# Kernel optimization log

Measured on AMD Instinct MI355X. Metric: run time of the kernel, lower is better.

Reference implementation:

```python
import jax, jax.numpy as jnp
import numpy as np


def setup_inputs() -> dict:
    key = jax.random.key(0)
    k1, k2, k3, k4 = jax.random.split(key, 4)
    T, IN, OUT = 4096, 4096, 4096  # tokens, in_features, out_features
    x = jax.random.normal(k1, (T, IN), dtype=jnp.float32)
    # simulated FP8 weight values (already quantized integers-ish codes stored as float)
    weight = jax.random.normal(k2, (OUT, IN), dtype=jnp.float32)
    # per-output-channel dequant scale
    weight_scale = jax.random.uniform(k3, (OUT,), dtype=jnp.float32, minval=0.01, maxval=0.1)
    bias = jax.random.normal(k4, (OUT,), dtype=jnp.float32)
    return {"x": x, "weight": weight, "weight_scale": weight_scale, "bias": bias}


def reference(x, weight, weight_scale, bias) -> jnp.ndarray:
    # FP8 quantized linear: dequantize weight with per-channel scale, then GEMM + bias.
    # weight: [out, in], weight_scale: [out], x: [tokens, in] -> out: [tokens, out]
    w_deq = weight * weight_scale[:, None]
    return jnp.einsum("ti,oi->to", x, w_deq) + bias
```

## Files before the change

### kernel.cpp

```cpp
#include <hip/hip_runtime.h>
#include <hip/hip_bf16.h>
#include <stdint.h>

typedef __bf16 bf16_t;
typedef bf16_t bf16x8 __attribute__((ext_vector_type(8)));
typedef float f32x4 __attribute__((ext_vector_type(4)));

#define BM 256
#define BN 256
#define BK 64

__device__ __forceinline__ void gload_lds16(const void* g, void* l) {
  __builtin_amdgcn_global_load_lds(
      (const __attribute__((address_space(1))) uint32_t*)g,
      (__attribute__((address_space(3))) uint32_t*)l, 16, 0, 0);
}

__global__ __launch_bounds__(256) void cvt_kernel(
    const float* __restrict__ x, bf16_t* __restrict__ xo, int n8x,
    const float* __restrict__ w, const float* __restrict__ scale,
    bf16_t* __restrict__ wo, int k8, int n8w, int gx) {
  if ((int)blockIdx.x < gx) {
    int stride = gx * blockDim.x;
    for (int i = blockIdx.x * blockDim.x + threadIdx.x; i < n8x; i += stride) {
      const f32x4* p = (const f32x4*)x + 2 * (size_t)i;
      f32x4 a = p[0], b = p[1];
      bf16x8 o;
#pragma unroll
      for (int r = 0; r < 4; ++r) { o[r] = (bf16_t)a[r]; o[r + 4] = (bf16_t)b[r]; }
      *((bf16x8*)xo + i) = o;
    }
  } else {
    int stride = (gridDim.x - gx) * blockDim.x;
    for (int i = (blockIdx.x - gx) * blockDim.x + threadIdx.x; i < n8w;
         i += stride) {
      int row = i / k8;
      float s = scale[row];
      const f32x4* p = (const f32x4*)w + 2 * (size_t)i;
      f32x4 a = p[0], b = p[1];
      bf16x8 o;
#pragma unroll
      for (int r = 0; r < 4; ++r) {
        o[r] = (bf16_t)(a[r] * s);
        o[r + 4] = (bf16_t)(b[r] * s);
      }
      *((bf16x8*)wo + i) = o;
    }
  }
}

__global__ __launch_bounds__(512, 2) void gemm256(
    const bf16_t* __restrict__ A, const bf16_t* __restrict__ B,
    const float* __restrict__ bias, float* __restrict__ C,
    int M, int N, int K) {
  __shared__ __attribute__((aligned(16))) char lds[131072];

  const int tid = threadIdx.x;
  const int lane = tid & 63;
  const int wave = tid >> 6;
  const int wm = wave >> 2;
  const int wn = wave & 3;

  int nwg = gridDim.x;
  int wg = blockIdx.x;
  if ((nwg & 7) == 0) { int cpx = nwg >> 3; wg = (wg & 7) * cpx + (wg >> 3); }
  const int ntn = N / BN;
  const int tm = wg / ntn;
  const int tn = wg % ntn;

  const size_t Kb = (size_t)K * 2;
  const char* gApan = (const char*)A + (size_t)tm * BM * Kb;
  const char* gBpan = (const char*)B + (size_t)tn * BN * Kb;

  const int xc = (((lane >> 4) ^ ((lane >> 1) & 3)) << 4);
  int aoff[2][4], boff[4];
#pragma unroll
  for (int ch = 0; ch < 2; ++ch)
#pragma unroll
    for (int i = 0; i < 4; ++i) {
      int row = wm * 128 + ch * 64 + i * 16 + (lane & 15);
      aoff[ch][i] = row * 64 + xc;
    }
#pragma unroll
  for (int j = 0; j < 4; ++j) {
    int row = wn * 64 + j * 16 + (lane & 15);
    boff[j] = row * 64 + xc;
  }

  size_t srcoff[2];
  int ldst[2];
#pragma unroll
  for (int s = 0; s < 2; ++s) {
    int r = (wave * 2 + s) * 16 + (lane >> 2);
    int c = (lane & 3) ^ ((lane >> 3) & 3);
    srcoff[s] = (size_t)r * Kb + (size_t)(c << 4);
    ldst[s] = (wave * 2 + s) * 1024;
  }

#define STAGE_U(dstbase, pan, kbyte)                                          \
  {                                                                           \
    gload_lds16((pan) + srcoff[0] + (size_t)(kbyte), lds + (dstbase) + ldst[0]); \
    gload_lds16((pan) + srcoff[1] + (size_t)(kbyte), lds + (dstbase) + ldst[1]); \
  }
#define RD_A(dst, base, ch)                                                   \
  _Pragma("unroll") for (int i_ = 0; i_ < 4; ++i_)                            \
      dst[i_] = *(const bf16x8*)((base) + aoff[ch][i_]);
#define RD_B(dst, base)                                                       \
  _Pragma("unroll") for (int j_ = 0; j_ < 4; ++j_)                            \
      dst[j_] = *(const bf16x8*)((base) + boff[j_]);
#define MFMA16(ab, bb_, accbase)                                              \
  __builtin_amdgcn_s_setprio(1);                                              \
  _Pragma("unroll") for (int i_ = 0; i_ < 4; ++i_)                            \
      _Pragma("unroll") for (int j_ = 0; j_ < 4; ++j_)                        \
          acc[(accbase) + i_][j_] = __builtin_amdgcn_mfma_f32_16x16x32_bf16(  \
              ab[i_], bb_[j_], acc[(accbase) + i_][j_], 0, 0, 0);             \
  __builtin_amdgcn_s_setprio(0);
#define WAIT_LGKM(n) asm volatile("s_waitcnt lgkmcnt(" #n ")" ::: "memory")
#define WAIT_VM(n)   asm volatile("s_waitcnt vmcnt(" #n ")" ::: "memory")
#define BAR()        __builtin_amdgcn_s_barrier()

  f32x4 acc[8][4];
#pragma unroll
  for (int a = 0; a < 8; ++a)
#pragma unroll
    for (int j = 0; j < 4; ++j) acc[a][j] = (f32x4)0.0f;

  const int NT = K / BK;

  STAGE_U(0,             gApan, 0);
  STAGE_U(32768,         gBpan, 0);
  STAGE_U(16384,         gApan, 64);
  STAGE_U(49152,         gBpan, 64);
  if (NT > 1) {
    STAGE_U(65536,         gApan, 128);
    STAGE_U(65536 + 32768, gBpan, 128);
    WAIT_VM(4);
  } else {
    WAIT_VM(0);
  }
  BAR();

  bf16x8 aX[4], aY[4], b0[4], b1[4];
  RD_A(aX, lds + 0, 0);
  RD_B(b0, lds + 32768);

  for (int t = 0; t < NT; ++t) {
    const int bb = (t & 1) << 16;
    const int nb = bb ^ 65536;
    const size_t kb1 = (size_t)(t + 1) * 128;
    const size_t kb2 = (size_t)(t + 2) * 128;
    const bool st1 = (t + 1) < NT;
    const bool st2 = (t + 2) < NT;

    const char* lA0 = lds + bb;
    const char* lA1 = lds + bb + 16384;
    const char* lB1 = lds + bb + 49152;

    RD_A(aY, lA0, 1);
    if (st1) STAGE_U(nb + 16384, gApan, kb1 + 64);
    WAIT_LGKM(4);
    MFMA16(aX, b0, 0);
    BAR();

    RD_A(aX, lA1, 0);
    RD_B(b1, lB1);
    if (st1) STAGE_U(nb + 49152, gBpan, kb1 + 64);
    WAIT_LGKM(8);
    MFMA16(aY, b0, 4);
    BAR();

    RD_A(aY, lA1, 1);
    if (st2) STAGE_U(bb, gApan, kb2);
    WAIT_LGKM(4);
    MFMA16(aX, b1, 0);
    WAIT_VM(6);
    BAR();

    if (st1) {
      RD_A(aX, lds + nb, 0);
      RD_B(b0, lds + nb + 32768);
    }
    if (st2) STAGE_U(bb + 32768, gBpan, kb2);
    if (st1) { WAIT_LGKM(8); } else { WAIT_LGKM(0); }
    MFMA16(aY, b1, 4);
    WAIT_VM(4);
    BAR();
  }
#undef STAGE_U
#undef RD_A
#undef RD_B
#undef MFMA16
#undef WAIT_LGKM
#undef WAIT_VM
#undef BAR

  const int row0 = tm * BM + wm * 128;
  const int col0 = tn * BN + wn * 64;
#pragma unroll
  for (int j = 0; j < 4; ++j) {
    int c = col0 + j * 16 + (lane & 15);
    float bv = bias[c];
#pragma unroll
    for (int a = 0; a < 8; ++a) {
      int ch = a >> 2, i = a & 3;
      int rbase = row0 + ch * 64 + i * 16 + ((lane >> 4) << 2);
#pragma unroll
      for (int r = 0; r < 4; ++r)
        C[(size_t)(rbase + r) * N + c] = acc[a][j][r] + bv;
    }
  }
}

__global__ void fallback_gemm(const float* __restrict__ x,
                              const float* __restrict__ w,
                              const float* __restrict__ s,
                              const float* __restrict__ b,
                              float* __restrict__ out, int M, int N, int K) {
  int o = blockIdx.x * blockDim.x + threadIdx.x;
  if (o >= M * N) return;
  int m = o / N, n = o % N;
  const float* xr = x + (size_t)m * K;
  const float* wr = w + (size_t)n * K;
  float acc = 0.f;
  for (int k = 0; k < K; ++k) acc += xr[k] * wr[k];
  out[o] = acc * s[n] + b[n];
}

extern "C" void kernel_launch(void* const* d_in, const int* in_sizes, int n_in,
                              void* d_out, int out_size, void* d_ws,
                              size_t ws_size, hipStream_t stream) {
  const float* x = (const float*)d_in[0];
  const float* w = (const float*)d_in[1];
  const float* sc = (const float*)d_in[2];
  const float* bias = (const float*)d_in[3];
  float* out = (float*)d_out;

  const int N = in_sizes[2];
  const int K = in_sizes[1] / N;
  const int M = in_sizes[0] / K;

  const size_t need = ((size_t)M * K + (size_t)N * K) * sizeof(bf16_t);
  const bool fast = (ws_size >= need) && (M % BM == 0) && (N % BN == 0) &&
                    (K % BK == 0) && (K / BK >= 1);

  if (fast) {
    bf16_t* xb = (bf16_t*)d_ws;
    bf16_t* wb = xb + (size_t)M * K;

    int n8x = (M * K) / 8;
    int n8w = (N * K) / 8;
    const int gx = 2048;
    cvt_kernel<<<gx + 2048, 256, 0, stream>>>(x, xb, n8x, w, sc, wb, K / 8,
                                              n8w, gx);

    dim3 grid((M / BM) * (N / BN));
    gemm256<<<grid, 512, 0, stream>>>(xb, wb, bias, out, M, N, K);
  } else {
    int total = M * N;
    fallback_gemm<<<(total + 255) / 256, 256, 0, stream>>>(x, w, sc, bias, out,
                                                           M, N, K);
  }
}
```

Measured before the change: 155.4 us.

## Replace double-buffered LDS fragment registers with single buffers and immediate offsets

```diff
diff --git a/kernel.cpp b/kernel.cpp
--- a/kernel.cpp
+++ b/kernel.cpp
@@ -73,19 +73,8 @@
   const char* gBpan = (const char*)B + (size_t)tn * BN * Kb;
 
   const int xc = (((lane >> 4) ^ ((lane >> 1) & 3)) << 4);
-  int aoff[2][4], boff[4];
-#pragma unroll
-  for (int ch = 0; ch < 2; ++ch)
-#pragma unroll
-    for (int i = 0; i < 4; ++i) {
-      int row = wm * 128 + ch * 64 + i * 16 + (lane & 15);
-      aoff[ch][i] = row * 64 + xc;
-    }
-#pragma unroll
-  for (int j = 0; j < 4; ++j) {
-    int row = wn * 64 + j * 16 + (lane & 15);
-    boff[j] = row * 64 + xc;
-  }
+  const int aBase = (wm * 128 + (lane & 15)) * 64 + xc;
+  const int bBase = (wn * 64 + (lane & 15)) * 64 + xc;
 
   size_t srcoff[2];
   int ldst[2];
@@ -102,12 +91,13 @@
     gload_lds16((pan) + srcoff[0] + (size_t)(kbyte), lds + (dstbase) + ldst[0]); \
     gload_lds16((pan) + srcoff[1] + (size_t)(kbyte), lds + (dstbase) + ldst[1]); \
   }
-#define RD_A(dst, base, ch)                                                   \
+#define RD_A(dst, unitbase, ch)                                               \
   _Pragma("unroll") for (int i_ = 0; i_ < 4; ++i_)                            \
-      dst[i_] = *(const bf16x8*)((base) + aoff[ch][i_]);
-#define RD_B(dst, base)                                                       \
+      dst[i_] = *(const bf16x8*)(lds + (unitbase) + aBase + (ch) * 4096 +     \
+                                 i_ * 1024);
+#define RD_B(dst, unitbase)                                                   \
   _Pragma("unroll") for (int j_ = 0; j_ < 4; ++j_)                            \
-      dst[j_] = *(const bf16x8*)((base) + boff[j_]);
+      dst[j_] = *(const bf16x8*)(lds + (unitbase) + bBase + j_ * 1024);
 #define MFMA16(ab, bb_, accbase)                                              \
   __builtin_amdgcn_s_setprio(1);                                              \
   _Pragma("unroll") for (int i_ = 0; i_ < 4; ++i_)                            \
@@ -115,7 +105,7 @@
           acc[(accbase) + i_][j_] = __builtin_amdgcn_mfma_f32_16x16x32_bf16(  \
               ab[i_], bb_[j_], acc[(accbase) + i_][j_], 0, 0, 0);             \
   __builtin_amdgcn_s_setprio(0);
-#define WAIT_LGKM(n) asm volatile("s_waitcnt lgkmcnt(" #n ")" ::: "memory")
+#define WAIT_LGKM0() asm volatile("s_waitcnt lgkmcnt(0)" ::: "memory")
 #define WAIT_VM(n)   asm volatile("s_waitcnt vmcnt(" #n ")" ::: "memory")
 #define BAR()        __builtin_amdgcn_s_barrier()
 
@@ -140,9 +130,7 @@
   }
   BAR();
 
-  bf16x8 aX[4], aY[4], b0[4], b1[4];
-  RD_A(aX, lds + 0, 0);
-  RD_B(b0, lds + 32768);
+  bf16x8 af[4], bf[4];
 
   for (int t = 0; t < NT; ++t) {
     const int bb = (t & 1) << 16;
@@ -152,45 +140,42 @@
     const bool st1 = (t + 1) < NT;
     const bool st2 = (t + 2) < NT;
 
-    const char* lA0 = lds + bb;
-    const char* lA1 = lds + bb + 16384;
-    const char* lB1 = lds + bb + 49152;
-
-    RD_A(aY, lA0, 1);
+    RD_A(af, bb, 0);
+    RD_B(bf, bb + 32768);
     if (st1) STAGE_U(nb + 16384, gApan, kb1 + 64);
-    WAIT_LGKM(4);
-    MFMA16(aX, b0, 0);
-    BAR();
-
-    RD_A(aX, lA1, 0);
-    RD_B(b1, lB1);
+    BAR();
+    WAIT_LGKM0();
+    MFMA16(af, bf, 0);
+    BAR();
+
+    RD_A(af, bb, 1);
     if (st1) STAGE_U(nb + 49152, gBpan, kb1 + 64);
-    WAIT_LGKM(8);
-    MFMA16(aY, b0, 4);
-    BAR();
-
-    RD_A(aY, lA1, 1);
+    BAR();
+    WAIT_LGKM0();
+    MFMA16(af, bf, 4);
+    BAR();
+
+    RD_A(af, bb + 16384, 0);
+    RD_B(bf, bb + 49152);
     if (st2) STAGE_U(bb, gApan, kb2);
-    WAIT_LGKM(4);
-    MFMA16(aX, b1, 0);
-    WAIT_VM(6);
-    BAR();
-
-    if (st1) {
-      RD_A(aX, lds + nb, 0);
-      RD_B(b0, lds + nb + 32768);
-    }
+    BAR();
+    WAIT_LGKM0();
+    MFMA16(af, bf, 0);
+    BAR();
+
+    RD_A(af, bb + 16384, 1);
     if (st2) STAGE_U(bb + 32768, gBpan, kb2);
-    if (st1) { WAIT_LGKM(8); } else { WAIT_LGKM(0); }
-    MFMA16(aY, b1, 4);
-    WAIT_VM(4);
+    BAR();
+    WAIT_LGKM0();
+    MFMA16(af, bf, 4);
+    if (st2) { WAIT_VM(4); } else { WAIT_VM(0); }
     BAR();
   }
 #undef STAGE_U
 #undef RD_A
 #undef RD_B
 #undef MFMA16
-#undef WAIT_LGKM
+#undef WAIT_LGKM0
 #undef WAIT_VM
 #undef BAR
 
```

Measured after the change: 158.9 us. +2.2%, slower.
